# Kernel optimization log

Measured on AMD Instinct MI355X. Metric: run time of the kernel, lower is better.

## Reference

```python
import jax, jax.numpy as jnp
import numpy as np

N, E, D = 50000, 600000, 128
EPS = 1e-8
BALL_EPS = 1e-5  # keep norms strictly < 1 for artanh


def _logmap0(x):
    # Poincare ball, c=1: logmap0(x) = artanh(||x||) * x / ||x||
    nrm = jnp.linalg.norm(x, axis=-1, keepdims=True)
    nrm_c = jnp.clip(nrm, EPS, 1.0 - BALL_EPS)
    return jnp.arctanh(nrm_c) * x / nrm_c


def _expmap0(v):
    # Poincare ball, c=1: expmap0(v) = tanh(||v||) * v / ||v||
    nrm = jnp.linalg.norm(v, axis=-1, keepdims=True)
    nrm_c = jnp.maximum(nrm, EPS)
    return jnp.tanh(nrm_c) * v / nrm_c


def setup_inputs() -> dict:
    key = jax.random.key(0)
    ks = jax.random.split(key, 7)
    # node features scaled to lie well inside the unit ball (valid Poincare points)
    x = jax.random.normal(ks[0], (N, D), dtype=jnp.float32) * 0.01
    edge_index = jax.random.randint(ks[1], (2, E), 0, N, dtype=jnp.int32)
    s = 1.0 / np.sqrt(D)
    w_msg1 = jax.random.normal(ks[2], (D, D), dtype=jnp.float32) * s
    w_msg2 = jax.random.normal(ks[3], (D, D), dtype=jnp.float32) * s
    w_upd1 = jax.random.normal(ks[4], (D, D), dtype=jnp.float32) * s
    w_upd2 = jax.random.normal(ks[5], (D, D), dtype=jnp.float32) * s
    b = lambda: jnp.zeros((D,), dtype=jnp.float32)
    return {"x": x, "edge_index": edge_index,
            "w_msg1": w_msg1, "b_msg1": b(), "w_msg2": w_msg2, "b_msg2": b(),
            "w_upd1": w_upd1, "b_upd1": b(), "w_upd2": w_upd2, "b_upd2": b()}


def reference(x, edge_index, w_msg1, b_msg1, w_msg2, b_msg2,
              w_upd1, b_upd1, w_upd2, b_upd2):
    x_t = _logmap0(x)                                  # [N, D]
    row, col = edge_index[0], edge_index[1]            # dst, src
    h = x_t[col]                                       # gather [E, D]
    msgs = jax.nn.relu(h @ w_msg1 + b_msg1) @ w_msg2 + b_msg2   # [E, D]
    # mean aggregation: scatter-add then divide by in-degree
    summed = jax.ops.segment_sum(msgs, row, num_segments=N)      # [N, D]
    count = jax.ops.segment_sum(jnp.ones((E,), dtype=jnp.float32), row, num_segments=N)
    out = summed / (count[:, None] + EPS)
    out = jax.nn.relu(out @ w_upd1 + b_upd1) @ w_upd2 + b_upd2
    return _expmap0(out)
```

## Files before the change

kernel.cpp:

```cpp
#include <hip/hip_runtime.h>
#include <hip/hip_bf16.h>


#define DD 128
#define CAP 64
#define DS 16

typedef __attribute__((ext_vector_type(8))) short short8;
typedef __attribute__((ext_vector_type(8))) unsigned short u16x8;
typedef __attribute__((ext_vector_type(4))) unsigned short u16x4;
typedef __attribute__((ext_vector_type(4))) float f32x4;

__device__ __forceinline__ unsigned short f2bf(float f) {
  unsigned u = __float_as_uint(f);
  u += 0x7fffu + ((u >> 16) & 1u);
  return (unsigned short)(u >> 16);
}
__device__ __forceinline__ float bf2f(short h) {
  return __uint_as_float(((unsigned)(unsigned short)h) << 16);
}

__global__ void k_init(const float* __restrict__ w1, const float* __restrict__ w2,
                       const float* __restrict__ w3, const float* __restrict__ w4,
                       unsigned short* __restrict__ P, int* __restrict__ degv, int N) {
  if (blockIdx.x < 32) {
    int idx = blockIdx.x * 256 + threadIdx.x;
    int m = idx >> 11;
    int id = idx & 2047;
    int f = id >> 6, l = id & 63;
    int cc = f >> 2, s = f & 3, q = l >> 4, n15 = l & 15;
    const float* W = (m == 0) ? w1 : (m == 1) ? w2 : (m == 2) ? w3 : w4;
    const float* wp = W + (s * 32 + q * 8) * DD + cc * 16 + n15;
    unsigned short* op = P + (size_t)m * 16384 + (size_t)id * 8;
#pragma unroll
    for (int j = 0; j < 8; ++j) op[j] = f2bf(wp[j * DD]);
  } else {
    int i = (blockIdx.x - 32) * 256 + threadIdx.x;
    if (i < N) degv[(size_t)i * DS] = 0;
  }
}

__global__ __launch_bounds__(256) void k_stage1(
    const float* __restrict__ x, const int* __restrict__ ei,
    const unsigned short* __restrict__ Pa, const float* __restrict__ ba,
    const unsigned short* __restrict__ Pb, const float* __restrict__ bb,
    unsigned short* __restrict__ node_msg, int* __restrict__ degv,
    unsigned short* __restrict__ ebuf, int N, int E, int ne) {
  __shared__ unsigned short As[32 * 136];
  const int tid = threadIdx.x;

  if (blockIdx.x < ne) {
    int eb_[4], d_[4], s_[4], p_[4];
#pragma unroll
    for (int k = 0; k < 4; ++k) {
      int e = blockIdx.x * 1024 + k * 256 + tid;
      eb_[k] = e;
      if (e < E) {
        d_[k] = ei[e];
        s_[k] = ei[E + e];
      }
    }
#pragma unroll
    for (int k = 0; k < 4; ++k)
      if (eb_[k] < E) p_[k] = atomicAdd(degv + (size_t)d_[k] * DS, 1);
#pragma unroll
    for (int k = 0; k < 4; ++k)
      if (eb_[k] < E && p_[k] < CAP)
        ebuf[(size_t)d_[k] * CAP + p_[k]] = (unsigned short)s_[k];
    return;
  }

  const int lane = tid & 63;
  const int wv = tid >> 6;
  const int rt = wv >> 1;
  const int ct = wv & 1;
  const int q = lane >> 4;
  const int n15 = lane & 15;
  const int row0 = (blockIdx.x - ne) * 32;
  const int g = (wv << 2) | q;

  f32x4 xa[2][2];
#pragma unroll
  for (int i = 0; i < 2; ++i) {
    const int grow = row0 + g * 2 + i;
    if (grow < N) {
      const f32x4* p = (const f32x4*)(x + (size_t)grow * DD + n15 * 8);
      xa[i][0] = p[0];
      xa[i][1] = p[1];
    } else {
      xa[i][0] = (f32x4){0.f, 0.f, 0.f, 0.f};
      xa[i][1] = (f32x4){0.f, 0.f, 0.f, 0.f};
    }
  }
#pragma unroll
  for (int i = 0; i < 2; ++i) {
    const int r = g * 2 + i;
    f32x4 s0 = xa[i][0], s1 = xa[i][1];
    float ss = s0[0]*s0[0] + s0[1]*s0[1] + s0[2]*s0[2] + s0[3]*s0[3]
             + s1[0]*s1[0] + s1[1]*s1[1] + s1[2]*s1[2] + s1[3]*s1[3];
    ss += __shfl_xor(ss, 1);
    ss += __shfl_xor(ss, 2);
    ss += __shfl_xor(ss, 4);
    ss += __shfl_xor(ss, 8);
    float nrm = sqrtf(ss);
    float nc = fminf(fmaxf(nrm, 1e-8f), 1.0f - 1e-5f);
    float sc = atanhf(nc) / nc;
    s0 *= sc;
    s1 *= sc;
    uint4 pk;
    pk.x = (unsigned)f2bf(s0[0]) | ((unsigned)f2bf(s0[1]) << 16);
    pk.y = (unsigned)f2bf(s0[2]) | ((unsigned)f2bf(s0[3]) << 16);
    pk.z = (unsigned)f2bf(s1[0]) | ((unsigned)f2bf(s1[1]) << 16);
    pk.w = (unsigned)f2bf(s1[2]) | ((unsigned)f2bf(s1[3]) << 16);
    *(uint4*)((unsigned*)As + r * 68 + n15 * 4) = pk;
  }
  __syncthreads();

  float bc[4];
#pragma unroll
  for (int c = 0; c < 4; ++c) bc[c] = ba[ct * 64 + c * 16 + n15];
  f32x4 acc[4];
#pragma unroll
  for (int c = 0; c < 4; ++c) acc[c] = (f32x4){0.f, 0.f, 0.f, 0.f};
  const int abase = (rt * 16 + n15) * 136 + q * 8;
  short8 bfr[16];
#pragma unroll
  for (int s = 0; s < 4; ++s)
#pragma unroll
    for (int c = 0; c < 4; ++c)
      bfr[s * 4 + c] =
          *(const short8*)&Pa[(size_t)(((((ct << 2) | c) << 2) | s) * 64 + lane) * 8];
  short8 afr[4];
#pragma unroll
  for (int s = 0; s < 4; ++s) afr[s] = *(const short8*)&As[abase + s * 32];
#pragma unroll
  for (int s = 0; s < 4; ++s)
#pragma unroll
    for (int c = 0; c < 4; ++c)
      acc[c] = __builtin_amdgcn_mfma_f32_16x16x32_bf16(afr[s], bfr[s * 4 + c],
                                                       acc[c], 0, 0, 0);
  __syncthreads();

#pragma unroll
  for (int c = 0; c < 4; ++c)
#pragma unroll
    for (int rr = 0; rr < 4; ++rr) {
      float v = fmaxf(acc[c][rr] + bc[c], 0.f);
      As[(rt * 16 + q * 4 + rr) * 136 + ct * 64 + c * 16 + n15] = f2bf(v);
    }
  __syncthreads();

#pragma unroll
  for (int c = 0; c < 4; ++c) bc[c] = bb[ct * 64 + c * 16 + n15];
#pragma unroll
  for (int c = 0; c < 4; ++c) acc[c] = (f32x4){0.f, 0.f, 0.f, 0.f};
#pragma unroll
  for (int s = 0; s < 4; ++s)
#pragma unroll
    for (int c = 0; c < 4; ++c)
      bfr[s * 4 + c] =
          *(const short8*)&Pb[(size_t)(((((ct << 2) | c) << 2) | s) * 64 + lane) * 8];
#pragma unroll
  for (int s = 0; s < 4; ++s) afr[s] = *(const short8*)&As[abase + s * 32];
#pragma unroll
  for (int s = 0; s < 4; ++s)
#pragma unroll
    for (int c = 0; c < 4; ++c)
      acc[c] = __builtin_amdgcn_mfma_f32_16x16x32_bf16(afr[s], bfr[s * 4 + c],
                                                       acc[c], 0, 0, 0);

  __syncthreads();
#pragma unroll
  for (int c = 0; c < 4; ++c)
#pragma unroll
    for (int rr = 0; rr < 4; ++rr)
      As[(rt * 16 + q * 4 + rr) * 136 + ct * 64 + c * 16 + n15] =
          f2bf(acc[c][rr] + bc[c]);
  __syncthreads();
#pragma unroll
  for (int k = 0; k < 2; ++k) {
    int u = tid + k * 256;
    int r = u >> 4, ch = u & 15;
    int grow = row0 + r;
    if (grow < N)
      *(short8*)(node_msg + (size_t)grow * DD + ch * 8) =
          *(const short8*)&As[r * 136 + ch * 8];
  }
}

__global__ __launch_bounds__(256) void k_stage2(
    const unsigned short* __restrict__ node_msg, const int* __restrict__ degv,
    const unsigned short* __restrict__ ebuf, const unsigned short* __restrict__ Pa,
    const float* __restrict__ ba, const unsigned short* __restrict__ Pb,
    const float* __restrict__ bb, float* __restrict__ out, int N) {
  __shared__ unsigned short As[32 * 136];
  __shared__ float nrmb[64];
  const int tid = threadIdx.x;
  const int lane = tid & 63;
  const int wv = tid >> 6;
  const int rt = wv >> 1;
  const int ct = wv & 1;
  const int q = lane >> 4;
  const int n15 = lane & 15;
  const int row0 = blockIdx.x * 32;
  const int g = (wv << 2) | q;

  int dpre[2];
#pragma unroll
  for (int i = 0; i < 2; ++i) {
    int grow = row0 + g * 2 + i;
    dpre[i] = (grow < N) ? degv[(size_t)grow * DS] : 0;
  }

#pragma unroll
  for (int i = 0; i < 2; ++i) {
    const int r = g * 2 + i;
    const int grow = row0 + r;
    f32x4 s0 = {0.f, 0.f, 0.f, 0.f}, s1 = {0.f, 0.f, 0.f, 0.f};
    if (grow < N) {
      const int d = dpre[i];
      const int dl = (d < CAP) ? d : CAP;
      const unsigned short* eb = ebuf + (size_t)grow * CAP;
      u16x8 cA = *(const u16x8*)(eb);
      u16x8 cB = *(const u16x8*)(eb + 8);
      int id[16];
#pragma unroll
      for (int t = 0; t < 8; ++t) {
        id[t] = cA[t];
        id[t + 8] = cB[t];
      }
      short8 v[16];
#pragma unroll
      for (int t = 0; t < 16; ++t) {
        int sidx = (t < dl) ? id[t] : 0;
        v[t] = *(const short8*)(node_msg + (size_t)sidx * DD + n15 * 8);
      }
      f32x4 t0 = {0.f, 0.f, 0.f, 0.f}, t1 = {0.f, 0.f, 0.f, 0.f};
#pragma unroll
      for (int t = 0; t < 16; ++t) {
        if (t < dl) {
#pragma unroll
          for (int j = 0; j < 4; ++j) {
            if (t & 1) {
              t0[j] += bf2f(v[t][j]);
              t1[j] += bf2f(v[t][j + 4]);
            } else {
              s0[j] += bf2f(v[t][j]);
              s1[j] += bf2f(v[t][j + 4]);
            }
          }
        }
      }
      int t = 16;
      for (; t + 3 < dl; t += 4) {
        u16x4 idx = *(const u16x4*)(eb + t);
        short8 v0 = *(const short8*)(node_msg + (size_t)idx[0] * DD + n15 * 8);
        short8 v1 = *(const short8*)(node_msg + (size_t)idx[1] * DD + n15 * 8);
        short8 v2 = *(const short8*)(node_msg + (size_t)idx[2] * DD + n15 * 8);
        short8 v3 = *(const short8*)(node_msg + (size_t)idx[3] * DD + n15 * 8);
#pragma unroll
        for (int j = 0; j < 4; ++j) {
          s0[j] += bf2f(v0[j]) + bf2f(v1[j]);
          s1[j] += bf2f(v0[j + 4]) + bf2f(v1[j + 4]);
          t0[j] += bf2f(v2[j]) + bf2f(v3[j]);
          t1[j] += bf2f(v2[j + 4]) + bf2f(v3[j + 4]);
        }
      }
      for (; t < dl; ++t) {
        int sa = eb[t];
        short8 va = *(const short8*)(node_msg + (size_t)sa * DD + n15 * 8);
#pragma unroll
        for (int j = 0; j < 4; ++j) {
          s0[j] += bf2f(va[j]);
          s1[j] += bf2f(va[j + 4]);
        }
      }
      s0 += t0;
      s1 += t1;
      float inv = 1.f / ((float)d + 1e-8f);
      s0 *= inv;
      s1 *= inv;
    }
    uint4 pk;
    pk.x = (unsigned)f2bf(s0[0]) | ((unsigned)f2bf(s0[1]) << 16);
    pk.y = (unsigned)f2bf(s0[2]) | ((unsigned)f2bf(s0[3]) << 16);
    pk.z = (unsigned)f2bf(s1[0]) | ((unsigned)f2bf(s1[1]) << 16);
    pk.w = (unsigned)f2bf(s1[2]) | ((unsigned)f2bf(s1[3]) << 16);
    *(uint4*)((unsigned*)As + r * 68 + n15 * 4) = pk;
  }
  __syncthreads();

  float bc[4];
#pragma unroll
  for (int c = 0; c < 4; ++c) bc[c] = ba[ct * 64 + c * 16 + n15];
  f32x4 acc[4];
#pragma unroll
  for (int c = 0; c < 4; ++c) acc[c] = (f32x4){0.f, 0.f, 0.f, 0.f};
  const int abase = (rt * 16 + n15) * 136 + q * 8;
  short8 bfr[16];
#pragma unroll
  for (int s = 0; s < 4; ++s)
#pragma unroll
    for (int c = 0; c < 4; ++c)
      bfr[s * 4 + c] =
          *(const short8*)&Pa[(size_t)(((((ct << 2) | c) << 2) | s) * 64 + lane) * 8];
  short8 afr[4];
#pragma unroll
  for (int s = 0; s < 4; ++s) afr[s] = *(const short8*)&As[abase + s * 32];
#pragma unroll
  for (int s = 0; s < 4; ++s)
#pragma unroll
    for (int c = 0; c < 4; ++c)
      acc[c] = __builtin_amdgcn_mfma_f32_16x16x32_bf16(afr[s], bfr[s * 4 + c],
                                                       acc[c], 0, 0, 0);
  __syncthreads();

#pragma unroll
  for (int c = 0; c < 4; ++c)
#pragma unroll
    for (int rr = 0; rr < 4; ++rr) {
      float v = fmaxf(acc[c][rr] + bc[c], 0.f);
      As[(rt * 16 + q * 4 + rr) * 136 + ct * 64 + c * 16 + n15] = f2bf(v);
    }
  __syncthreads();

#pragma unroll
  for (int c = 0; c < 4; ++c) bc[c] = bb[ct * 64 + c * 16 + n15];
#pragma unroll
  for (int c = 0; c < 4; ++c) acc[c] = (f32x4){0.f, 0.f, 0.f, 0.f};
#pragma unroll
  for (int s = 0; s < 4; ++s)
#pragma unroll
    for (int c = 0; c < 4; ++c)
      bfr[s * 4 + c] =
          *(const short8*)&Pb[(size_t)(((((ct << 2) | c) << 2) | s) * 64 + lane) * 8];
#pragma unroll
  for (int s = 0; s < 4; ++s) afr[s] = *(const short8*)&As[abase + s * 32];
#pragma unroll
  for (int s = 0; s < 4; ++s)
#pragma unroll
    for (int c = 0; c < 4; ++c)
      acc[c] = __builtin_amdgcn_mfma_f32_16x16x32_bf16(afr[s], bfr[s * 4 + c],
                                                       acc[c], 0, 0, 0);

  float v[4][4];
#pragma unroll
  for (int rr = 0; rr < 4; ++rr) {
    float ssq = 0.f;
#pragma unroll
    for (int c = 0; c < 4; ++c) {
      v[c][rr] = acc[c][rr] + bc[c];
      ssq += v[c][rr] * v[c][rr];
    }
    ssq += __shfl_xor(ssq, 1);
    ssq += __shfl_xor(ssq, 2);
    ssq += __shfl_xor(ssq, 4);
    ssq += __shfl_xor(ssq, 8);
    if (n15 == 0) nrmb[(rt * 16 + q * 4 + rr) * 2 + ct] = ssq;
  }
  __syncthreads();
#pragma unroll
  for (int rr = 0; rr < 4; ++rr) {
    int r = rt * 16 + q * 4 + rr;
    int grow = row0 + r;
    float ssq = nrmb[r * 2] + nrmb[r * 2 + 1];
    float nrm = sqrtf(ssq);
    float nc = fmaxf(nrm, 1e-8f);
    float sc = tanhf(nc) / nc;
    if (grow < N) {
#pragma unroll
      for (int c = 0; c < 4; ++c)
        __builtin_nontemporal_store(
            v[c][rr] * sc, out + (size_t)grow * DD + ct * 64 + c * 16 + n15);
    }
  }
}

extern "C" void kernel_launch(void* const* d_in, const int* in_sizes, int n_in,
                              void* d_out, int out_size, void* d_ws, size_t ws_size,
                              hipStream_t stream) {
  const float* x = (const float*)d_in[0];
  const int* ei = (const int*)d_in[1];
  const float* w1 = (const float*)d_in[2];
  const float* b1 = (const float*)d_in[3];
  const float* w2 = (const float*)d_in[4];
  const float* b2 = (const float*)d_in[5];
  const float* w3 = (const float*)d_in[6];
  const float* b3 = (const float*)d_in[7];
  const float* w4 = (const float*)d_in[8];
  const float* b4 = (const float*)d_in[9];
  const int N = in_sizes[0] / DD;
  const int E = in_sizes[1] / 2;
  const int nf = (N + 31) / 32;
  const int ne = (E + 1023) / 1024;

  unsigned short* node_msg = (unsigned short*)d_ws;
  int* degv = (int*)(node_msg + (size_t)N * DD);
  unsigned short* ebuf = (unsigned short*)(degv + (size_t)N * DS);
  uintptr_t pw = (uintptr_t)(ebuf + (size_t)N * CAP);
  pw = (pw + 63) & ~(uintptr_t)63;
  unsigned short* P = (unsigned short*)pw;
  float* outp = (float*)d_out;

  hipLaunchKernelGGL(k_init, dim3(32 + (N + 255) / 256), dim3(256), 0, stream,
                     w1, w2, w3, w4, P, degv, N);
  hipLaunchKernelGGL(k_stage1, dim3(ne + nf), dim3(256), 0, stream,
                     x, ei, P, b1, P + 16384, b2, node_msg, degv, ebuf, N, E, ne);
  hipLaunchKernelGGL(k_stage2, dim3(nf), dim3(256), 0, stream,
                     node_msg, degv, ebuf, P + 2 * 16384, b3, P + 3 * 16384, b4,
                     outp, N);
}
```

Before: 158.2 us.

## Split per-node degree counters and edge buckets into eight replicated sub-buckets

Replaces the single padded per-node degree counter and 64-slot edge list with eight sub-buckets selected by edge-block index, each with its own dense counter array and 16-slot list. This spreads atomic contention across replicas and drops the 16x padding of counters. Stage 2 now reads eight counters and eight index vectors per node and gathers up to four neighbors per sub-bucket speculatively, then handles overflow serially. This adds more scattered metadata loads and wasted gathers for low-degree nodes. Per-node capacity grows from 64 to 128 edges in total, but any single sub-bucket is capped at 16.

```diff
diff --git a/kernel.cpp b/kernel.cpp
--- a/kernel.cpp
+++ b/kernel.cpp
@@ -3,8 +3,8 @@
 
 
 #define DD 128
-#define CAP 64
-#define DS 16
+#define CAP8 16
+#define NR 8
 
 typedef __attribute__((ext_vector_type(8))) short short8;
 typedef __attribute__((ext_vector_type(8))) unsigned short u16x8;
@@ -22,7 +22,7 @@
 
 __global__ void k_init(const float* __restrict__ w1, const float* __restrict__ w2,
                        const float* __restrict__ w3, const float* __restrict__ w4,
-                       unsigned short* __restrict__ P, int* __restrict__ degv, int N) {
+                       unsigned short* __restrict__ P, int* __restrict__ degv8, int N) {
   if (blockIdx.x < 32) {
     int idx = blockIdx.x * 256 + threadIdx.x;
     int m = idx >> 11;
@@ -36,7 +36,7 @@
     for (int j = 0; j < 8; ++j) op[j] = f2bf(wp[j * DD]);
   } else {
     int i = (blockIdx.x - 32) * 256 + threadIdx.x;
-    if (i < N) degv[(size_t)i * DS] = 0;
+    if (i < NR * N) degv8[i] = 0;
   }
 }
 
@@ -44,12 +44,13 @@
     const float* __restrict__ x, const int* __restrict__ ei,
     const unsigned short* __restrict__ Pa, const float* __restrict__ ba,
     const unsigned short* __restrict__ Pb, const float* __restrict__ bb,
-    unsigned short* __restrict__ node_msg, int* __restrict__ degv,
-    unsigned short* __restrict__ ebuf, int N, int E, int ne) {
+    unsigned short* __restrict__ node_msg, int* __restrict__ degv8,
+    unsigned short* __restrict__ ebuf8, int N, int E, int ne) {
   __shared__ unsigned short As[32 * 136];
   const int tid = threadIdx.x;
 
   if (blockIdx.x < ne) {
+    const int rg = blockIdx.x & (NR - 1);
     int eb_[4], d_[4], s_[4], p_[4];
 #pragma unroll
     for (int k = 0; k < 4; ++k) {
@@ -62,11 +63,12 @@
     }
 #pragma unroll
     for (int k = 0; k < 4; ++k)
-      if (eb_[k] < E) p_[k] = atomicAdd(degv + (size_t)d_[k] * DS, 1);
+      if (eb_[k] < E)
+        p_[k] = atomicAdd(degv8 + (size_t)rg * N + d_[k], 1);
 #pragma unroll
     for (int k = 0; k < 4; ++k)
-      if (eb_[k] < E && p_[k] < CAP)
-        ebuf[(size_t)d_[k] * CAP + p_[k]] = (unsigned short)s_[k];
+      if (eb_[k] < E && p_[k] < CAP8)
+        ebuf8[((size_t)rg * N + d_[k]) * CAP8 + p_[k]] = (unsigned short)s_[k];
     return;
   }
 
@@ -189,8 +191,8 @@
 }
 
 __global__ __launch_bounds__(256) void k_stage2(
-    const unsigned short* __restrict__ node_msg, const int* __restrict__ degv,
-    const unsigned short* __restrict__ ebuf, const unsigned short* __restrict__ Pa,
+    const unsigned short* __restrict__ node_msg, const int* __restrict__ degv8,
+    const unsigned short* __restrict__ ebuf8, const unsigned short* __restrict__ Pa,
     const float* __restrict__ ba, const unsigned short* __restrict__ Pb,
     const float* __restrict__ bb, float* __restrict__ out, int N) {
   __shared__ unsigned short As[32 * 136];
@@ -205,79 +207,75 @@
   const int row0 = blockIdx.x * 32;
   const int g = (wv << 2) | q;
 
-  int dpre[2];
-#pragma unroll
-  for (int i = 0; i < 2; ++i) {
-    int grow = row0 + g * 2 + i;
-    dpre[i] = (grow < N) ? degv[(size_t)grow * DS] : 0;
-  }
-
 #pragma unroll
   for (int i = 0; i < 2; ++i) {
     const int r = g * 2 + i;
     const int grow = row0 + r;
     f32x4 s0 = {0.f, 0.f, 0.f, 0.f}, s1 = {0.f, 0.f, 0.f, 0.f};
+    f32x4 t0 = {0.f, 0.f, 0.f, 0.f}, t1 = {0.f, 0.f, 0.f, 0.f};
+    int dtot = 0;
     if (grow < N) {
-      const int d = dpre[i];
-      const int dl = (d < CAP) ? d : CAP;
-      const unsigned short* eb = ebuf + (size_t)grow * CAP;
-      u16x8 cA = *(const u16x8*)(eb);
-      u16x8 cB = *(const u16x8*)(eb + 8);
-      int id[16];
-#pragma unroll
-      for (int t = 0; t < 8; ++t) {
-        id[t] = cA[t];
-        id[t + 8] = cB[t];
+      int d8[NR];
+#pragma unroll
+      for (int rg = 0; rg < NR; ++rg) d8[rg] = degv8[(size_t)rg * N + grow];
+      u16x4 cw[NR];
+#pragma unroll
+      for (int rg = 0; rg < NR; ++rg)
+        cw[rg] = *(const u16x4*)(ebuf8 + ((size_t)rg * N + grow) * CAP8);
+#pragma unroll
+      for (int rg = 0; rg < NR; ++rg) dtot += d8[rg];
+
+#pragma unroll
+      for (int h = 0; h < 2; ++h) {
+        short8 v[16];
+#pragma unroll
+        for (int rr8 = 0; rr8 < 4; ++rr8)
+#pragma unroll
+          for (int t = 0; t < 4; ++t) {
+            const int rg = h * 4 + rr8;
+            int sidx = (t < d8[rg]) ? (int)cw[rg][t] : 0;
+            v[rr8 * 4 + t] =
+                *(const short8*)(node_msg + (size_t)sidx * DD + n15 * 8);
+          }
+#pragma unroll
+        for (int rr8 = 0; rr8 < 4; ++rr8)
+#pragma unroll
+          for (int t = 0; t < 4; ++t) {
+            const int rg = h * 4 + rr8;
+            if (t < d8[rg]) {
+              const short8 vv = v[rr8 * 4 + t];
+#pragma unroll
+              for (int j = 0; j < 4; ++j) {
+                if (t & 1) {
+                  t0[j] += bf2f(vv[j]);
+                  t1[j] += bf2f(vv[j + 4]);
+                } else {
+                  s0[j] += bf2f(vv[j]);
+                  s1[j] += bf2f(vv[j + 4]);
+                }
+              }
+            }
+          }
       }
-      short8 v[16];
-#pragma unroll
-      for (int t = 0; t < 16; ++t) {
-        int sidx = (t < dl) ? id[t] : 0;
-        v[t] = *(const short8*)(node_msg + (size_t)sidx * DD + n15 * 8);
-      }
-      f32x4 t0 = {0.f, 0.f, 0.f, 0.f}, t1 = {0.f, 0.f, 0.f, 0.f};
-#pragma unroll
-      for (int t = 0; t < 16; ++t) {
-        if (t < dl) {
-#pragma unroll
-          for (int j = 0; j < 4; ++j) {
-            if (t & 1) {
-              t0[j] += bf2f(v[t][j]);
-              t1[j] += bf2f(v[t][j + 4]);
-            } else {
-              s0[j] += bf2f(v[t][j]);
-              s1[j] += bf2f(v[t][j + 4]);
+#pragma unroll
+      for (int rg = 0; rg < NR; ++rg) {
+        int dl = (d8[rg] < CAP8) ? d8[rg] : CAP8;
+        if (dl > 4) {
+          const unsigned short* eb = ebuf8 + ((size_t)rg * N + grow) * CAP8;
+          for (int t = 4; t < dl; ++t) {
+            int sa = eb[t];
+            short8 va = *(const short8*)(node_msg + (size_t)sa * DD + n15 * 8);
+#pragma unroll
+            for (int j = 0; j < 4; ++j) {
+              s0[j] += bf2f(va[j]);
+              s1[j] += bf2f(va[j + 4]);
             }
           }
         }
       }
-      int t = 16;
-      for (; t + 3 < dl; t += 4) {
-        u16x4 idx = *(const u16x4*)(eb + t);
-        short8 v0 = *(const short8*)(node_msg + (size_t)idx[0] * DD + n15 * 8);
-        short8 v1 = *(const short8*)(node_msg + (size_t)idx[1] * DD + n15 * 8);
-        short8 v2 = *(const short8*)(node_msg + (size_t)idx[2] * DD + n15 * 8);
-        short8 v3 = *(const short8*)(node_msg + (size_t)idx[3] * DD + n15 * 8);
-#pragma unroll
-        for (int j = 0; j < 4; ++j) {
-          s0[j] += bf2f(v0[j]) + bf2f(v1[j]);
-          s1[j] += bf2f(v0[j + 4]) + bf2f(v1[j + 4]);
-          t0[j] += bf2f(v2[j]) + bf2f(v3[j]);
-          t1[j] += bf2f(v2[j + 4]) + bf2f(v3[j + 4]);
-        }
-      }
-      for (; t < dl; ++t) {
-        int sa = eb[t];
-        short8 va = *(const short8*)(node_msg + (size_t)sa * DD + n15 * 8);
-#pragma unroll
-        for (int j = 0; j < 4; ++j) {
-          s0[j] += bf2f(va[j]);
-          s1[j] += bf2f(va[j + 4]);
-        }
-      }
       s0 += t0;
       s1 += t1;
-      float inv = 1.f / ((float)d + 1e-8f);
+      float inv = 1.f / ((float)dtot + 1e-8f);
       s0 *= inv;
       s1 *= inv;
     }
@@ -395,18 +393,18 @@
   const int ne = (E + 1023) / 1024;
 
   unsigned short* node_msg = (unsigned short*)d_ws;
-  int* degv = (int*)(node_msg + (size_t)N * DD);
-  unsigned short* ebuf = (unsigned short*)(degv + (size_t)N * DS);
-  uintptr_t pw = (uintptr_t)(ebuf + (size_t)N * CAP);
+  int* degv8 = (int*)(node_msg + (size_t)N * DD);
+  unsigned short* ebuf8 = (unsigned short*)(degv8 + (size_t)NR * N);
+  uintptr_t pw = (uintptr_t)(ebuf8 + (size_t)NR * N * CAP8);
   pw = (pw + 63) & ~(uintptr_t)63;
   unsigned short* P = (unsigned short*)pw;
   float* outp = (float*)d_out;
 
-  hipLaunchKernelGGL(k_init, dim3(32 + (N + 255) / 256), dim3(256), 0, stream,
-                     w1, w2, w3, w4, P, degv, N);
+  hipLaunchKernelGGL(k_init, dim3(32 + (NR * N + 255) / 256), dim3(256), 0,
+                     stream, w1, w2, w3, w4, P, degv8, N);
   hipLaunchKernelGGL(k_stage1, dim3(ne + nf), dim3(256), 0, stream,
-                     x, ei, P, b1, P + 16384, b2, node_msg, degv, ebuf, N, E, ne);
+                     x, ei, P, b1, P + 16384, b2, node_msg, degv8, ebuf8, N, E, ne);
   hipLaunchKernelGGL(k_stage2, dim3(nf), dim3(256), 0, stream,
-                     node_msg, degv, ebuf, P + 2 * 16384, b3, P + 3 * 16384, b4,
+                     node_msg, degv8, ebuf8, P + 2 * 16384, b3, P + 3 * 16384, b4,
                      outp, N);
 }
```

After: 166.0 us. 4.9% more time.

## Shrink stage2 to single-wave blocks of 16 rows covering all columns

Applied to the files above, without the earlier changes.

Restructures the aggregation-plus-update kernel so each block is one 64-lane wavefront handling 16 rows and all 128 output columns, instead of four waves splitting 32 rows by row and column tiles. This removes the cross-wave LDS norm reduction and its barrier, and makes the remaining syncthreads cheap within a single wave. Weight fragments are now loaded inside the MFMA loop rather than preloaded into registers. Each block does more gather and MFMA work per wave with four times as many blocks; the risk is less latency hiding per block and repeated weight loads from cache.

```diff
diff --git a/kernel.cpp b/kernel.cpp
--- a/kernel.cpp
+++ b/kernel.cpp
@@ -188,37 +188,24 @@
   }
 }
 
-__global__ __launch_bounds__(256) void k_stage2(
+__global__ __launch_bounds__(64) void k_stage2(
     const unsigned short* __restrict__ node_msg, const int* __restrict__ degv,
     const unsigned short* __restrict__ ebuf, const unsigned short* __restrict__ Pa,
     const float* __restrict__ ba, const unsigned short* __restrict__ Pb,
     const float* __restrict__ bb, float* __restrict__ out, int N) {
-  __shared__ unsigned short As[32 * 136];
-  __shared__ float nrmb[64];
-  const int tid = threadIdx.x;
-  const int lane = tid & 63;
-  const int wv = tid >> 6;
-  const int rt = wv >> 1;
-  const int ct = wv & 1;
+  __shared__ unsigned short As[16 * 136];
+  const int lane = threadIdx.x;
   const int q = lane >> 4;
   const int n15 = lane & 15;
-  const int row0 = blockIdx.x * 32;
-  const int g = (wv << 2) | q;
-
-  int dpre[2];
-#pragma unroll
-  for (int i = 0; i < 2; ++i) {
-    int grow = row0 + g * 2 + i;
-    dpre[i] = (grow < N) ? degv[(size_t)grow * DS] : 0;
-  }
-
-#pragma unroll
-  for (int i = 0; i < 2; ++i) {
-    const int r = g * 2 + i;
+  const int row0 = blockIdx.x * 16;
+
+#pragma unroll
+  for (int i = 0; i < 4; ++i) {
+    const int r = q * 4 + i;
     const int grow = row0 + r;
     f32x4 s0 = {0.f, 0.f, 0.f, 0.f}, s1 = {0.f, 0.f, 0.f, 0.f};
     if (grow < N) {
-      const int d = dpre[i];
+      const int d = degv[(size_t)grow * DS];
       const int dl = (d < CAP) ? d : CAP;
       const unsigned short* eb = ebuf + (size_t)grow * CAP;
       u16x8 cA = *(const u16x8*)(eb);
@@ -290,88 +277,70 @@
   }
   __syncthreads();
 
-  float bc[4];
-#pragma unroll
-  for (int c = 0; c < 4; ++c) bc[c] = ba[ct * 64 + c * 16 + n15];
-  f32x4 acc[4];
-#pragma unroll
-  for (int c = 0; c < 4; ++c) acc[c] = (f32x4){0.f, 0.f, 0.f, 0.f};
-  const int abase = (rt * 16 + n15) * 136 + q * 8;
-  short8 bfr[16];
-#pragma unroll
-  for (int s = 0; s < 4; ++s)
-#pragma unroll
-    for (int c = 0; c < 4; ++c)
-      bfr[s * 4 + c] =
-          *(const short8*)&Pa[(size_t)(((((ct << 2) | c) << 2) | s) * 64 + lane) * 8];
+  float bc[8];
+#pragma unroll
+  for (int cc = 0; cc < 8; ++cc) bc[cc] = ba[cc * 16 + n15];
+  f32x4 acc[8];
+#pragma unroll
+  for (int cc = 0; cc < 8; ++cc) acc[cc] = (f32x4){0.f, 0.f, 0.f, 0.f};
+  const int abase = n15 * 136 + q * 8;
   short8 afr[4];
 #pragma unroll
   for (int s = 0; s < 4; ++s) afr[s] = *(const short8*)&As[abase + s * 32];
 #pragma unroll
   for (int s = 0; s < 4; ++s)
 #pragma unroll
-    for (int c = 0; c < 4; ++c)
-      acc[c] = __builtin_amdgcn_mfma_f32_16x16x32_bf16(afr[s], bfr[s * 4 + c],
-                                                       acc[c], 0, 0, 0);
-  __syncthreads();
-
-#pragma unroll
-  for (int c = 0; c < 4; ++c)
+    for (int cc = 0; cc < 8; ++cc) {
+      short8 b = *(const short8*)&Pa[(size_t)((cc * 4 + s) * 64 + lane) * 8];
+      acc[cc] = __builtin_amdgcn_mfma_f32_16x16x32_bf16(afr[s], b, acc[cc], 0, 0, 0);
+    }
+  __syncthreads();
+
+#pragma unroll
+  for (int cc = 0; cc < 8; ++cc)
 #pragma unroll
     for (int rr = 0; rr < 4; ++rr) {
-      float v = fmaxf(acc[c][rr] + bc[c], 0.f);
-      As[(rt * 16 + q * 4 + rr) * 136 + ct * 64 + c * 16 + n15] = f2bf(v);
-    }
-  __syncthreads();
-
-#pragma unroll
-  for (int c = 0; c < 4; ++c) bc[c] = bb[ct * 64 + c * 16 + n15];
-#pragma unroll
-  for (int c = 0; c < 4; ++c) acc[c] = (f32x4){0.f, 0.f, 0.f, 0.f};
-#pragma unroll
-  for (int s = 0; s < 4; ++s)
-#pragma unroll
-    for (int c = 0; c < 4; ++c)
-      bfr[s * 4 + c] =
-          *(const short8*)&Pb[(size_t)(((((ct << 2) | c) << 2) | s) * 64 + lane) * 8];
+      float v = fmaxf(acc[cc][rr] + bc[cc], 0.f);
+      As[(q * 4 + rr) * 136 + cc * 16 + n15] = f2bf(v);
+    }
+  __syncthreads();
+
+#pragma unroll
+  for (int cc = 0; cc < 8; ++cc) bc[cc] = bb[cc * 16 + n15];
+#pragma unroll
+  for (int cc = 0; cc < 8; ++cc) acc[cc] = (f32x4){0.f, 0.f, 0.f, 0.f};
 #pragma unroll
   for (int s = 0; s < 4; ++s) afr[s] = *(const short8*)&As[abase + s * 32];
 #pragma unroll
   for (int s = 0; s < 4; ++s)
 #pragma unroll
-    for (int c = 0; c < 4; ++c)
-      acc[c] = __builtin_amdgcn_mfma_f32_16x16x32_bf16(afr[s], bfr[s * 4 + c],
-                                                       acc[c], 0, 0, 0);
-
-  float v[4][4];
+    for (int cc = 0; cc < 8; ++cc) {
+      short8 b = *(const short8*)&Pb[(size_t)((cc * 4 + s) * 64 + lane) * 8];
+      acc[cc] = __builtin_amdgcn_mfma_f32_16x16x32_bf16(afr[s], b, acc[cc], 0, 0, 0);
+    }
+
 #pragma unroll
   for (int rr = 0; rr < 4; ++rr) {
+    float vv[8];
     float ssq = 0.f;
 #pragma unroll
-    for (int c = 0; c < 4; ++c) {
-      v[c][rr] = acc[c][rr] + bc[c];
-      ssq += v[c][rr] * v[c][rr];
+    for (int cc = 0; cc < 8; ++cc) {
+      vv[cc] = acc[cc][rr] + bc[cc];
+      ssq += vv[cc] * vv[cc];
     }
     ssq += __shfl_xor(ssq, 1);
     ssq += __shfl_xor(ssq, 2);
     ssq += __shfl_xor(ssq, 4);
     ssq += __shfl_xor(ssq, 8);
-    if (n15 == 0) nrmb[(rt * 16 + q * 4 + rr) * 2 + ct] = ssq;
-  }
-  __syncthreads();
-#pragma unroll
-  for (int rr = 0; rr < 4; ++rr) {
-    int r = rt * 16 + q * 4 + rr;
-    int grow = row0 + r;
-    float ssq = nrmb[r * 2] + nrmb[r * 2 + 1];
     float nrm = sqrtf(ssq);
     float nc = fmaxf(nrm, 1e-8f);
     float sc = tanhf(nc) / nc;
+    int grow = row0 + q * 4 + rr;
     if (grow < N) {
 #pragma unroll
-      for (int c = 0; c < 4; ++c)
+      for (int cc = 0; cc < 8; ++cc)
         __builtin_nontemporal_store(
-            v[c][rr] * sc, out + (size_t)grow * DD + ct * 64 + c * 16 + n15);
+            vv[cc] * sc, out + (size_t)grow * DD + cc * 16 + n15);
     }
   }
 }
@@ -392,6 +361,7 @@
   const int N = in_sizes[0] / DD;
   const int E = in_sizes[1] / 2;
   const int nf = (N + 31) / 32;
+  const int nf2 = (N + 15) / 16;
   const int ne = (E + 1023) / 1024;
 
   unsigned short* node_msg = (unsigned short*)d_ws;
@@ -406,7 +376,7 @@
                      w1, w2, w3, w4, P, degv, N);
   hipLaunchKernelGGL(k_stage1, dim3(ne + nf), dim3(256), 0, stream,
                      x, ei, P, b1, P + 16384, b2, node_msg, degv, ebuf, N, E, ne);
-  hipLaunchKernelGGL(k_stage2, dim3(nf), dim3(256), 0, stream,
+  hipLaunchKernelGGL(k_stage2, dim3(nf2), dim3(64), 0, stream,
                      node_msg, degv, ebuf, P + 2 * 16384, b3, P + 3 * 16384, b4,
                      outp, N);
 }
```

New measurement: 155.6 us. About the same (-1.7%).
